# Kernel optimization log

Hardware: AMD Instinct MI355X
Metric: run time of the kernel (lower is better)

Reference implementation:

```python
import jax, jax.numpy as jnp
import numpy as np


def setup_inputs() -> dict:
    key = jax.random.key(0)
    ks = jax.random.split(key, 4)
    B, T, I, H = 64, 1024, 256, 512
    s = 1.0 / np.sqrt(I + H)  # torch Linear default init scale
    xs = jax.random.normal(ks[0], (B, T, I), dtype=jnp.float32)
    Wz = jax.random.uniform(ks[1], (I + H, H), jnp.float32, -s, s)
    Wr = jax.random.uniform(ks[2], (I + H, H), jnp.float32, -s, s)
    Wh = jax.random.uniform(ks[3], (I + H, H), jnp.float32, -s, s)
    bz = jnp.zeros((H,), jnp.float32)
    br = jnp.zeros((H,), jnp.float32)
    bh = jnp.zeros((H,), jnp.float32)
    return {"xs": xs, "Wz": Wz, "bz": bz, "Wr": Wr, "br": br, "Wh": Wh, "bh": bh}


def reference(xs, Wz, bz, Wr, br, Wh, bh):
    B, T, I = xs.shape
    H = Wz.shape[1]
    # split weights into input / hidden blocks so per-step work avoids concat
    Wz_x, Wz_h = Wz[:I], Wz[I:]
    Wr_x, Wr_h = Wr[:I], Wr[I:]
    Wh_x, Wh_h = Wh[:I], Wh[I:]
    # precompute all input projections in one big GEMM per gate: [B,T,H]
    xz = jnp.einsum('bti,ih->bth', xs, Wz_x) + bz
    xr = jnp.einsum('bti,ih->bth', xs, Wr_x) + br
    xh = jnp.einsum('bti,ih->bth', xs, Wh_x) + bh

    def step(h, inp):
        xz_t, xr_t, xh_t = inp
        zt = jax.nn.sigmoid(xz_t + h @ Wz_h)
        rt = jax.nn.sigmoid(xr_t + h @ Wr_h)
        ht = jnp.tanh(xh_t + (rt * h) @ Wh_h)
        h_next = (1 - zt) * h + zt * ht
        return h_next, h_next

    h0 = jnp.zeros((B, H), xs.dtype)
    # scan over time: inputs as [T, B, H]
    xs_t = (jnp.swapaxes(xz, 0, 1), jnp.swapaxes(xr, 0, 1), jnp.swapaxes(xh, 0, 1))
    h_last, hs = jax.lax.scan(step, h0, xs_t)
    return jnp.swapaxes(hs, 0, 1), h_last
```

## Files before the change

kernel.cpp:

```cpp
#include <hip/hip_runtime.h>
#include <cmath>

typedef __bf16 bf16x8 __attribute__((ext_vector_type(8)));
typedef float  f32x4  __attribute__((ext_vector_type(4)));
typedef unsigned long long u64;
typedef u64 u64x2 __attribute__((ext_vector_type(2)));

#define T_STEPS 1024
#define I_DIM   256
#define H_DIM   512
#define B_TOT   64
#define NBT     4
#define NCT     32
#define BT      16
#define CT      16
#define FPAD    16

__device__ __forceinline__ f32x4 mfma16(bf16x8 a, bf16x8 b, f32x4 c) {
    return __builtin_amdgcn_mfma_f32_16x16x32_bf16(a, b, c, 0, 0, 0);
}

__device__ __forceinline__ bf16x8 cvt8(const float* p) {
    float4 a = *(const float4*)p;
    float4 b = *(const float4*)(p + 4);
    bf16x8 f;
    f[0] = (__bf16)a.x; f[1] = (__bf16)a.y; f[2] = (__bf16)a.z; f[3] = (__bf16)a.w;
    f[4] = (__bf16)b.x; f[5] = (__bf16)b.y; f[6] = (__bf16)b.z; f[7] = (__bf16)b.w;
    return f;
}

__device__ __forceinline__ int ld_flag(const int* p) {
    return __hip_atomic_load(p, __ATOMIC_RELAXED, __HIP_MEMORY_SCOPE_AGENT);
}
__device__ __forceinline__ void st_flag(int* p, int v) {
    __hip_atomic_store(p, v, __ATOMIC_RELAXED, __HIP_MEMORY_SCOPE_AGENT);
}
__device__ __forceinline__ void st_u32(unsigned* p, unsigned v) {
    __hip_atomic_store(p, v, __ATOMIC_RELAXED, __HIP_MEMORY_SCOPE_AGENT);
}
__device__ __forceinline__ bf16x8 ld_frag16(const __bf16* p) {
    u64x2 v;
    v.x = __hip_atomic_load((const u64*)p,     __ATOMIC_RELAXED, __HIP_MEMORY_SCOPE_AGENT);
    v.y = __hip_atomic_load((const u64*)p + 1, __ATOMIC_RELAXED, __HIP_MEMORY_SCOPE_AGENT);
    return __builtin_bit_cast(bf16x8, v);
}

__device__ __forceinline__ void wait128(const int* fb, int target) {
    const int l = threadIdx.x & 63;
    const int* p0 = fb + l * FPAD;
    const int* p1 = fb + (l + 64) * FPAD;
    for (int g = 0; g < (1 << 22); ++g) {
        int a = ld_flag(p0);
        int b = ld_flag(p1);
        if (__ballot(a >= target && b >= target) == ~0ull) break;
    }
    asm volatile("" ::: "memory");
}

__device__ __forceinline__ void drain_stores() {
    __builtin_amdgcn_s_waitcnt(0x0f70);
}

__global__ __launch_bounds__(256, 1) void gru_persist(
    const float* __restrict__ xs,
    const float* __restrict__ Wz, const float* __restrict__ bz,
    const float* __restrict__ Wr, const float* __restrict__ br,
    const float* __restrict__ Wh, const float* __restrict__ bh,
    float* __restrict__ out,
    __bf16* hbuf, __bf16* rhbuf, int* flag_h, int* flag_r)
{
    const int bid  = blockIdx.x;
    const int i    = bid & (NBT - 1);
    const int j    = bid >> 2;
    const int tid  = threadIdx.x;
    const int w    = tid >> 6;
    const int lane = tid & 63;
    const int q    = lane >> 4;
    const int ln   = lane & 15;
    const int cb   = j * CT;

    __shared__ float red1[2][4][16][17];
    __shared__ float red2[4][16][17];
    __shared__ float z_lds[16][17];

    bf16x8 BZ[6], BR[6], BH[6];
    #pragma unroll
    for (int s = 0; s < 6; ++s) {
        int kk = w + 4 * s;
        int krow = kk * 32 + q * 8;
        bf16x8 fz, fr, fh;
        #pragma unroll
        for (int jj = 0; jj < 8; ++jj) {
            int off = (krow + jj) * H_DIM + cb + ln;
            fz[jj] = (__bf16)Wz[off];
            fr[jj] = (__bf16)Wr[off];
            fh[jj] = (__bf16)Wh[off];
        }
        BZ[s] = fz; BR[s] = fr; BH[s] = fh;
    }

    const int m = tid >> 4;
    const int c = tid & 15;
    const float bzc = bz[cb + c], brc = br[cb + c], bhc = bh[cb + c];
    float hprev = 0.0f;

    const float* xrow = xs + (size_t)(i * BT + ln) * T_STEPS * I_DIM;
    const int HB_P = NBT * BT * H_DIM;
    int* fh_dom = flag_h + i * (NCT * 4) * FPAD;
    int* fr_dom = flag_r + i * (NCT * 4) * FPAD;
    int* my_fh  = fh_dom + (j * 4 + w) * FPAD;
    int* my_fr  = fr_dom + (j * 4 + w) * FPAD;

    for (int t = 0; t < T_STEPS; ++t) {
        const int p = t & 1, pp = p ^ 1;
        f32x4 accz = {0,0,0,0}, accr = {0,0,0,0}, acch = {0,0,0,0};

        const float* xt = xrow + (size_t)t * I_DIM;
        #pragma unroll
        for (int s = 0; s < 2; ++s) {
            int kk = w + 4 * s;
            bf16x8 ax = cvt8(xt + kk * 32 + q * 8);
            accz = mfma16(ax, BZ[s], accz);
            accr = mfma16(ax, BR[s], accr);
            acch = mfma16(ax, BH[s], acch);
        }

        if (t > 0) wait128(fh_dom, t);

        const __bf16* hb = hbuf + pp * HB_P + i * (BT * H_DIM) + ln * H_DIM;
        #pragma unroll
        for (int s = 2; s < 6; ++s) {
            int kk = w + 4 * s;
            bf16x8 ah = ld_frag16(hb + (kk - 8) * 32 + q * 8);
            accz = mfma16(ah, BZ[s], accz);
            accr = mfma16(ah, BR[s], accr);
        }

        #pragma unroll
        for (int r4 = 0; r4 < 4; ++r4) {
            red1[0][w][q*4 + r4][ln] = accz[r4];
            red1[1][w][q*4 + r4][ln] = accr[r4];
        }
        __syncthreads();

        {
            float pz = red1[0][0][m][c] + red1[0][1][m][c] + red1[0][2][m][c] + red1[0][3][m][c] + bzc;
            float pr = red1[1][0][m][c] + red1[1][1][m][c] + red1[1][2][m][c] + red1[1][3][m][c] + brc;
            float zv = 1.0f / (1.0f + __expf(-pz));
            float rv = 1.0f / (1.0f + __expf(-pr));
            z_lds[m][c] = zv;
            unsigned short v16 = __builtin_bit_cast(unsigned short, (__bf16)(rv * hprev));
            unsigned short nb  = (unsigned short)__shfl((int)v16, lane + 1);
            if (!(c & 1)) {
                unsigned pkd = (unsigned)v16 | ((unsigned)nb << 16);
                st_u32((unsigned*)(rhbuf + p * HB_P + i * (BT * H_DIM) + m * H_DIM + cb + c), pkd);
            }
            drain_stores();
            if (lane == 0) st_flag(my_fr, t + 1);
        }

        wait128(fr_dom, t + 1);

        const __bf16* rb = rhbuf + p * HB_P + i * (BT * H_DIM) + ln * H_DIM;
        #pragma unroll
        for (int s = 2; s < 6; ++s) {
            int kk = w + 4 * s;
            bf16x8 ar = ld_frag16(rb + (kk - 8) * 32 + q * 8);
            acch = mfma16(ar, BH[s], acch);
        }

        #pragma unroll
        for (int r4 = 0; r4 < 4; ++r4)
            red2[w][q*4 + r4][ln] = acch[r4];
        __syncthreads();

        {
            float ph  = red2[0][m][c] + red2[1][m][c] + red2[2][m][c] + red2[3][m][c] + bhc;
            float e2  = __expf(2.0f * ph);
            float htl = (e2 - 1.0f) / (e2 + 1.0f);
            float zv2 = z_lds[m][c];
            float hn  = (1.0f - zv2) * hprev + zv2 * htl;
            hprev = hn;

            int bglob = i * BT + m;
            out[((size_t)bglob * T_STEPS + t) * H_DIM + cb + c] = hn;
            if (t == T_STEPS - 1)
                out[(size_t)B_TOT * T_STEPS * H_DIM + (size_t)bglob * H_DIM + cb + c] = hn;

            unsigned short v16 = __builtin_bit_cast(unsigned short, (__bf16)hn);
            unsigned short nb  = (unsigned short)__shfl((int)v16, lane + 1);
            if (!(c & 1)) {
                unsigned pkd = (unsigned)v16 | ((unsigned)nb << 16);
                st_u32((unsigned*)(hbuf + p * HB_P + i * (BT * H_DIM) + m * H_DIM + cb + c), pkd);
            }
            drain_stores();
            if (lane == 0) st_flag(my_fh, t + 1);
        }
    }
}

extern "C" void kernel_launch(void* const* d_in, const int* in_sizes, int n_in,
                              void* d_out, int out_size, void* d_ws, size_t ws_size,
                              hipStream_t stream)
{
    const float* xs = (const float*)d_in[0];
    const float* Wz = (const float*)d_in[1];
    const float* bz = (const float*)d_in[2];
    const float* Wr = (const float*)d_in[3];
    const float* br = (const float*)d_in[4];
    const float* Wh = (const float*)d_in[5];
    const float* bh = (const float*)d_in[6];
    float* out = (float*)d_out;

    __bf16* hbuf  = (__bf16*)d_ws;
    __bf16* rhbuf = hbuf + 2 * NBT * BT * H_DIM;
    int* flag_h = (int*)((char*)d_ws + 262144);
    int* flag_r = flag_h + NBT * NCT * 4 * FPAD;

    hipMemsetAsync(d_ws, 0, 262144 + 2 * NBT * NCT * 4 * FPAD * 4, stream);
    gru_persist<<<dim3(NBT * NCT), dim3(256), 0, stream>>>(
        xs, Wz, bz, Wr, br, Wh, bh, out, hbuf, rhbuf, flag_h, flag_r);
}
```

Baseline: 6.441 ms.

## Use per-block packed flags, prefetch next-step inputs, and defer output stores past flag

Replaces the 128 padded per-wave flags in each batch domain with 32 contiguous per-block flags. A block barrier now comes before a single thread publishes, so waiters poll one cacheline with one load per lane instead of two scattered loads. The x row for step t+1 is loaded into registers one step ahead, which hides global load latency behind the recurrent work. The large output store is moved after the h flag publication, so its drain no longer delays the signal. The trade-off is an extra __syncthreads per phase and contention on a shared flag cacheline.

```diff
diff --git a/kernel.cpp b/kernel.cpp
--- a/kernel.cpp
+++ b/kernel.cpp
@@ -14,15 +14,13 @@
 #define NCT     32
 #define BT      16
 #define CT      16
-#define FPAD    16
+#define FDOM    64
 
 __device__ __forceinline__ f32x4 mfma16(bf16x8 a, bf16x8 b, f32x4 c) {
     return __builtin_amdgcn_mfma_f32_16x16x32_bf16(a, b, c, 0, 0, 0);
 }
 
-__device__ __forceinline__ bf16x8 cvt8(const float* p) {
-    float4 a = *(const float4*)p;
-    float4 b = *(const float4*)(p + 4);
+__device__ __forceinline__ bf16x8 cvt8r(float4 a, float4 b) {
     bf16x8 f;
     f[0] = (__bf16)a.x; f[1] = (__bf16)a.y; f[2] = (__bf16)a.z; f[3] = (__bf16)a.w;
     f[4] = (__bf16)b.x; f[5] = (__bf16)b.y; f[6] = (__bf16)b.z; f[7] = (__bf16)b.w;
@@ -45,19 +43,16 @@
     return __builtin_bit_cast(bf16x8, v);
 }
 
-__device__ __forceinline__ void wait128(const int* fb, int target) {
-    const int l = threadIdx.x & 63;
-    const int* p0 = fb + l * FPAD;
-    const int* p1 = fb + (l + 64) * FPAD;
+__device__ __forceinline__ void wait32(const int* fdom, int target) {
+    const int* p = fdom + (threadIdx.x & 31);
     for (int g = 0; g < (1 << 22); ++g) {
-        int a = ld_flag(p0);
-        int b = ld_flag(p1);
-        if (__ballot(a >= target && b >= target) == ~0ull) break;
+        int v = ld_flag(p);
+        if (__ballot(v >= target) == ~0ull) break;
     }
     asm volatile("" ::: "memory");
 }
 
-__device__ __forceinline__ void drain_stores() {
+__device__ __forceinline__ void drain_vm() {
     __builtin_amdgcn_s_waitcnt(0x0f70);
 }
 
@@ -106,26 +101,47 @@
 
     const float* xrow = xs + (size_t)(i * BT + ln) * T_STEPS * I_DIM;
     const int HB_P = NBT * BT * H_DIM;
-    int* fh_dom = flag_h + i * (NCT * 4) * FPAD;
-    int* fr_dom = flag_r + i * (NCT * 4) * FPAD;
-    int* my_fh  = fh_dom + (j * 4 + w) * FPAD;
-    int* my_fr  = fr_dom + (j * 4 + w) * FPAD;
+    int* fh_dom = flag_h + i * FDOM;
+    int* fr_dom = flag_r + i * FDOM;
+    int* my_fh  = fh_dom + j;
+    int* my_fr  = fr_dom + j;
+
+    float4 xr[4];
+    {
+        const float* x0 = xrow;
+        xr[0] = *(const float4*)(x0 + (w    ) * 32 + q * 8);
+        xr[1] = *(const float4*)(x0 + (w    ) * 32 + q * 8 + 4);
+        xr[2] = *(const float4*)(x0 + (w + 4) * 32 + q * 8);
+        xr[3] = *(const float4*)(x0 + (w + 4) * 32 + q * 8 + 4);
+    }
 
     for (int t = 0; t < T_STEPS; ++t) {
         const int p = t & 1, pp = p ^ 1;
+
+        float4 xn[4];
+        {
+            int tn = (t + 1 < T_STEPS) ? t + 1 : t;
+            const float* xp = xrow + (size_t)tn * I_DIM;
+            xn[0] = *(const float4*)(xp + (w    ) * 32 + q * 8);
+            xn[1] = *(const float4*)(xp + (w    ) * 32 + q * 8 + 4);
+            xn[2] = *(const float4*)(xp + (w + 4) * 32 + q * 8);
+            xn[3] = *(const float4*)(xp + (w + 4) * 32 + q * 8 + 4);
+        }
+
         f32x4 accz = {0,0,0,0}, accr = {0,0,0,0}, acch = {0,0,0,0};
 
-        const float* xt = xrow + (size_t)t * I_DIM;
-        #pragma unroll
-        for (int s = 0; s < 2; ++s) {
-            int kk = w + 4 * s;
-            bf16x8 ax = cvt8(xt + kk * 32 + q * 8);
-            accz = mfma16(ax, BZ[s], accz);
-            accr = mfma16(ax, BR[s], accr);
-            acch = mfma16(ax, BH[s], acch);
-        }
-
-        if (t > 0) wait128(fh_dom, t);
+        {
+            bf16x8 ax0 = cvt8r(xr[0], xr[1]);
+            bf16x8 ax1 = cvt8r(xr[2], xr[3]);
+            accz = mfma16(ax0, BZ[0], accz);
+            accr = mfma16(ax0, BR[0], accr);
+            acch = mfma16(ax0, BH[0], acch);
+            accz = mfma16(ax1, BZ[1], accz);
+            accr = mfma16(ax1, BR[1], accr);
+            acch = mfma16(ax1, BH[1], acch);
+        }
+
+        if (t > 0) wait32(fh_dom, t);
 
         const __bf16* hb = hbuf + pp * HB_P + i * (BT * H_DIM) + ln * H_DIM;
         #pragma unroll
@@ -155,11 +171,12 @@
                 unsigned pkd = (unsigned)v16 | ((unsigned)nb << 16);
                 st_u32((unsigned*)(rhbuf + p * HB_P + i * (BT * H_DIM) + m * H_DIM + cb + c), pkd);
             }
-            drain_stores();
-            if (lane == 0) st_flag(my_fr, t + 1);
-        }
-
-        wait128(fr_dom, t + 1);
+            drain_vm();
+            __syncthreads();
+            if (tid == 0) st_flag(my_fr, t + 1);
+        }
+
+        wait32(fr_dom, t + 1);
 
         const __bf16* rb = rhbuf + p * HB_P + i * (BT * H_DIM) + ln * H_DIM;
         #pragma unroll
@@ -182,20 +199,23 @@
             float hn  = (1.0f - zv2) * hprev + zv2 * htl;
             hprev = hn;
 
-            int bglob = i * BT + m;
-            out[((size_t)bglob * T_STEPS + t) * H_DIM + cb + c] = hn;
-            if (t == T_STEPS - 1)
-                out[(size_t)B_TOT * T_STEPS * H_DIM + (size_t)bglob * H_DIM + cb + c] = hn;
-
             unsigned short v16 = __builtin_bit_cast(unsigned short, (__bf16)hn);
             unsigned short nb  = (unsigned short)__shfl((int)v16, lane + 1);
             if (!(c & 1)) {
                 unsigned pkd = (unsigned)v16 | ((unsigned)nb << 16);
                 st_u32((unsigned*)(hbuf + p * HB_P + i * (BT * H_DIM) + m * H_DIM + cb + c), pkd);
             }
-            drain_stores();
-            if (lane == 0) st_flag(my_fh, t + 1);
-        }
+            drain_vm();
+            __syncthreads();
+            if (tid == 0) st_flag(my_fh, t + 1);
+
+            int bglob = i * BT + m;
+            out[((size_t)bglob * T_STEPS + t) * H_DIM + cb + c] = hn;
+            if (t == T_STEPS - 1)
+                out[(size_t)B_TOT * T_STEPS * H_DIM + (size_t)bglob * H_DIM + cb + c] = hn;
+        }
+
+        xr[0] = xn[0]; xr[1] = xn[1]; xr[2] = xn[2]; xr[3] = xn[3];
     }
 }
 
@@ -215,9 +235,9 @@
     __bf16* hbuf  = (__bf16*)d_ws;
     __bf16* rhbuf = hbuf + 2 * NBT * BT * H_DIM;
     int* flag_h = (int*)((char*)d_ws + 262144);
-    int* flag_r = flag_h + NBT * NCT * 4 * FPAD;
-
-    hipMemsetAsync(d_ws, 0, 262144 + 2 * NBT * NCT * 4 * FPAD * 4, stream);
+    int* flag_r = flag_h + NBT * FDOM;
+
+    hipMemsetAsync(d_ws, 0, 262144 + 2 * NBT * FDOM * 4, stream);
     gru_persist<<<dim3(NBT * NCT), dim3(256), 0, stream>>>(
         xs, Wz, bz, Wr, br, Wh, bh, out, hbuf, rhbuf, flag_h, flag_r);
 }
```

After: 6.138 ms. 4.7% less time.
